# Optimization experiments

Measured on AMD Instinct MI355X. Metric: run time of the kernel, lower is better.

Reference implementation:

```python
import jax, jax.numpy as jnp
import numpy as np

MOD_EMBED_DIM = 16
HIDDEN = 64
NUM_MODALITIES = 3
MLP_IN = 2 + 2 * MOD_EMBED_DIM + 2  # 36


def setup_inputs() -> dict:
    key = jax.random.key(0)
    ks = jax.random.split(key, 4)
    h, w = 40, 40
    return {
        "h": h,
        "w": w,
        "q_mod": 0,
        "k_mod": 2,
        "structure_map": jax.random.normal(ks[0], (4, 1, 80, 80), jnp.float32),
        "mod_embed": jax.random.normal(ks[1], (NUM_MODALITIES, MOD_EMBED_DIM), jnp.float32),
        "W1": jax.random.normal(ks[2], (MLP_IN, HIDDEN), jnp.float32) * 0.1,
        "b1": jnp.zeros((HIDDEN,), jnp.float32),
        "W2": jax.random.normal(ks[3], (HIDDEN, 1), jnp.float32) * 0.1,
        "b2": jnp.zeros((1,), jnp.float32),
    }


def reference(h, w, q_mod, k_mod, structure_map, mod_embed, W1, b1, W2, b2):
    # --- coords on a [-0.5, 0.5] grid, flattened row-major -> (N, 2) as (x, y)
    ys = jnp.linspace(-0.5, 0.5, h)
    xs = jnp.linspace(-0.5, 0.5, w)
    yy, xx = jnp.meshgrid(ys, xs, indexing="ij")
    coords = jnp.stack([xx, yy], axis=-1).reshape(-1, 2)  # (N, 2)
    N = coords.shape[0]

    # relative coords per pair (i, j): (N, N, 2)
    rel = coords[:, None, :] - coords[None, :, :]

    # modality pair embedding: constant across all pairs -> (2*E,)
    mod_vec = jnp.concatenate([mod_embed[q_mod], mod_embed[k_mod]])

    # structure: bilinear resize to (h, w) (half-pixel == align_corners=False),
    # then mean over batch -> per-position scalar s_mean: (N,)
    b = structure_map.shape[0]
    s = jax.image.resize(structure_map, (b, 1, h, w), method="linear")
    s_mean = s.reshape(-1, 1, N)[:, 0, :].mean(axis=0)  # (N,)

    # First linear layer applied to the (implicit) concat
    # [rel, mod_vec, s_i, s_j] by splitting W1 — same math as concat @ W1,
    # but avoids materializing the (N^2, 36) concat tensor.
    W_rel = W1[:2]            # (2, H)
    W_mod = W1[2:2 + 2 * MOD_EMBED_DIM]  # (32, H)
    W_si = W1[-2]             # (H,)
    W_sj = W1[-1]             # (H,)

    hid = (
        jnp.einsum("ijc,ch->ijh", rel, W_rel)
        + (mod_vec @ W_mod + b1)
        + s_mean[:, None, None] * W_si
        + s_mean[None, :, None] * W_sj
    )  # (N, N, H)
    hid = jax.nn.relu(hid)
    bias = jnp.einsum("ijh,ho->ijo", hid, W2) + b2  # (N, N, 1)
    return bias.reshape(1, 1, N, N)
```

## Files before the change

kernel.cpp:

```cpp
#include <hip/hip_runtime.h>

#define HIN  80
#define WIN  80
#define NB   4
#define HOUT 40
#define WOUT 40
#define NPTS (HOUT*WOUT)
#define NHID 64

__global__ __launch_bounds__(64) void rpe_setup(
    const int* __restrict__ qmod, const int* __restrict__ kmod,
    const float* __restrict__ smap, const float* __restrict__ mode,
    const float* __restrict__ W1, const float* __restrict__ b1,
    float* __restrict__ Arows, float* __restrict__ Crows)
{
    __shared__ float wr0[NHID], wr1[NHID], wsi[NHID], wsj[NHID], sbase[NHID];
    __shared__ float smn[64], pxs[64], pys[64];
    const int t = threadIdx.x;

    wr0[t] = W1[t];
    wr1[t] = W1[NHID + t];
    wsi[t] = W1[34*NHID + t];
    wsj[t] = W1[35*NHID + t];
    const int q = qmod[0], k = kmod[0];
    float bacc = b1[t];
    #pragma unroll
    for (int m = 0; m < 16; ++m) bacc += mode[q*16 + m] * W1[(2 + m)*NHID + t];
    #pragma unroll
    for (int m = 0; m < 16; ++m) bacc += mode[k*16 + m] * W1[(18 + m)*NHID + t];
    sbase[t] = bacc;

    const int p  = blockIdx.x * 64 + t;
    const int oy = p / WOUT, ox = p % WOUT;
    float wy[4], wx[4]; int iy[4], ix[4];
    float wsy = 0.f, wsx = 0.f;
    #pragma unroll
    for (int d = 0; d < 4; ++d) {
        const float wv = (d == 0 || d == 3) ? 0.25f : 0.75f;
        const int yi = 2*oy + d - 1;
        const int xi = 2*ox + d - 1;
        iy[d] = yi < 0 ? 0 : (yi >= HIN ? HIN - 1 : yi);
        ix[d] = xi < 0 ? 0 : (xi >= WIN ? WIN - 1 : xi);
        wy[d] = (yi >= 0 && yi < HIN) ? wv : 0.f;
        wx[d] = (xi >= 0 && xi < WIN) ? wv : 0.f;
        wsy += wy[d]; wsx += wx[d];
    }
    float acc = 0.f;
    for (int b = 0; b < NB; ++b) {
        const float* bp = smap + b*HIN*WIN;
        #pragma unroll
        for (int dy = 0; dy < 4; ++dy) {
            const float* rp = bp + iy[dy]*WIN;
            float rs = 0.f;
            #pragma unroll
            for (int dx = 0; dx < 4; ++dx) rs += wx[dx] * rp[ix[dx]];
            acc += wy[dy] * rs;
        }
    }
    const float smean = acc / (wsy * wsx * (float)NB);
    smn[t] = smean;
    pxs[t] = -0.5f + (float)ox * (1.0f/(float)(WOUT-1));
    pys[t] = -0.5f + (float)oy * (1.0f/(float)(HOUT-1));
    __syncthreads();

    const float w0 = wr0[t], w1v = wr1[t], wiv = wsi[t], wjv = wsj[t], bb = sbase[t];
    const int pbase = blockIdx.x * 64;
    for (int pl = 0; pl < 64; ++pl) {
        const float lin = pxs[pl]*w0 + pys[pl]*w1v;
        const float s   = smn[pl];
        Arows[(pbase + pl)*NHID + t] =  lin + s*wiv + bb;
        Crows[(pbase + pl)*NHID + t] = -lin + s*wjv;
    }
}

__global__ __launch_bounds__(256) void rpe_bias(
    const float* __restrict__ Arows, const float* __restrict__ Crows,
    const float* __restrict__ W2, const float* __restrict__ b2,
    float* __restrict__ out)
{
    __shared__ float As[64][68];
    __shared__ float Cs[64][68];
    __shared__ float w2s[NHID];
    const int t  = threadIdx.x;
    const int bi = blockIdx.y, bj = blockIdx.x;

    #pragma unroll
    for (int k = 0; k < 4; ++k) {
        const int idx = t + k*256;
        const int row = idx >> 4;
        const int col = (idx & 15) << 2;
        const float4 av = *(const float4*)(Arows + (size_t)(bi*64 + row)*NHID + col);
        const float4 cv = *(const float4*)(Crows + (size_t)(bj*64 + row)*NHID + col);
        *(float4*)&As[row][col] = av;
        *(float4*)&Cs[row][col] = cv;
    }
    if (t < NHID) w2s[t] = W2[t];
    __syncthreads();

    const int tx = t & 15;
    const int ty = t >> 4;

    float4 acc[4][4];
    #pragma unroll
    for (int ii = 0; ii < 4; ++ii)
        #pragma unroll
        for (int jj = 0; jj < 4; ++jj) acc[ii][jj] = make_float4(0.f, 0.f, 0.f, 0.f);

    #pragma unroll
    for (int h = 0; h < NHID; h += 4) {
        const float4 w4 = *(const float4*)&w2s[h];
        float4 a[4], c[4];
        #pragma unroll
        for (int ii = 0; ii < 4; ++ii) a[ii] = *(const float4*)&As[ty + ii*16][h];
        #pragma unroll
        for (int jj = 0; jj < 4; ++jj) c[jj] = *(const float4*)&Cs[tx + jj*16][h];
        #pragma unroll
        for (int ii = 0; ii < 4; ++ii) {
            #pragma unroll
            for (int jj = 0; jj < 4; ++jj) {
                float4 v;
                v.x = fmaxf(a[ii].x + c[jj].x, 0.f);
                v.y = fmaxf(a[ii].y + c[jj].y, 0.f);
                v.z = fmaxf(a[ii].z + c[jj].z, 0.f);
                v.w = fmaxf(a[ii].w + c[jj].w, 0.f);
                acc[ii][jj].x = fmaf(v.x, w4.x, acc[ii][jj].x);
                acc[ii][jj].y = fmaf(v.y, w4.y, acc[ii][jj].y);
                acc[ii][jj].z = fmaf(v.z, w4.z, acc[ii][jj].z);
                acc[ii][jj].w = fmaf(v.w, w4.w, acc[ii][jj].w);
            }
        }
    }

    const float bias2 = b2[0];
    #pragma unroll
    for (int ii = 0; ii < 4; ++ii) {
        const int i = bi*64 + ty + ii*16;
        float* orow = out + (size_t)i*NPTS + bj*64;
        #pragma unroll
        for (int jj = 0; jj < 4; ++jj) {
            const float4 a4 = acc[ii][jj];
            orow[tx + jj*16] = (a4.x + a4.y) + (a4.z + a4.w) + bias2;
        }
    }
}

extern "C" void kernel_launch(void* const* d_in, const int* in_sizes, int n_in,
                              void* d_out, int out_size, void* d_ws, size_t ws_size,
                              hipStream_t stream) {
    const int*   qm   = (const int*)d_in[2];
    const int*   km   = (const int*)d_in[3];
    const float* smap = (const float*)d_in[4];
    const float* mode = (const float*)d_in[5];
    const float* W1   = (const float*)d_in[6];
    const float* b1   = (const float*)d_in[7];
    const float* W2   = (const float*)d_in[8];
    const float* b2   = (const float*)d_in[9];
    float* out = (float*)d_out;

    float* Arows = (float*)d_ws;
    float* Crows = Arows + (size_t)NPTS * NHID;

    rpe_setup<<<NPTS/64, 64, 0, stream>>>(qm, km, smap, mode, W1, b1, Arows, Crows);
    rpe_bias<<<dim3(NPTS/64, NPTS/64), 256, 0, stream>>>(Arows, Crows, W2, b2, out);
}
```

Baseline: 93.10 us.

## Fuse setup into bias kernel, recomputing A/C rows per tile in shared memory

Merges the setup kernel into the bias kernel. Each 64x64 tile block now computes its own resized structure means, coordinates and first-layer partial rows directly into shared memory, instead of reading precomputed A/C rows from a workspace. This removes one kernel launch and the global round trip through the workspace. In exchange, every block redundantly recomputes the bilinear resize and the modality bias, which adds gather loads of the structure map and extra prologue latency per block.

```diff
diff --git a/kernel.cpp b/kernel.cpp
--- a/kernel.cpp
+++ b/kernel.cpp
@@ -8,97 +8,90 @@
 #define NPTS (HOUT*WOUT)
 #define NHID 64
 
-__global__ __launch_bounds__(64) void rpe_setup(
+__global__ __launch_bounds__(256) void rpe_fused(
     const int* __restrict__ qmod, const int* __restrict__ kmod,
     const float* __restrict__ smap, const float* __restrict__ mode,
     const float* __restrict__ W1, const float* __restrict__ b1,
-    float* __restrict__ Arows, float* __restrict__ Crows)
-{
-    __shared__ float wr0[NHID], wr1[NHID], wsi[NHID], wsj[NHID], sbase[NHID];
-    __shared__ float smn[64], pxs[64], pys[64];
-    const int t = threadIdx.x;
-
-    wr0[t] = W1[t];
-    wr1[t] = W1[NHID + t];
-    wsi[t] = W1[34*NHID + t];
-    wsj[t] = W1[35*NHID + t];
-    const int q = qmod[0], k = kmod[0];
-    float bacc = b1[t];
-    #pragma unroll
-    for (int m = 0; m < 16; ++m) bacc += mode[q*16 + m] * W1[(2 + m)*NHID + t];
-    #pragma unroll
-    for (int m = 0; m < 16; ++m) bacc += mode[k*16 + m] * W1[(18 + m)*NHID + t];
-    sbase[t] = bacc;
-
-    const int p  = blockIdx.x * 64 + t;
-    const int oy = p / WOUT, ox = p % WOUT;
-    float wy[4], wx[4]; int iy[4], ix[4];
-    float wsy = 0.f, wsx = 0.f;
-    #pragma unroll
-    for (int d = 0; d < 4; ++d) {
-        const float wv = (d == 0 || d == 3) ? 0.25f : 0.75f;
-        const int yi = 2*oy + d - 1;
-        const int xi = 2*ox + d - 1;
-        iy[d] = yi < 0 ? 0 : (yi >= HIN ? HIN - 1 : yi);
-        ix[d] = xi < 0 ? 0 : (xi >= WIN ? WIN - 1 : xi);
-        wy[d] = (yi >= 0 && yi < HIN) ? wv : 0.f;
-        wx[d] = (xi >= 0 && xi < WIN) ? wv : 0.f;
-        wsy += wy[d]; wsx += wx[d];
-    }
-    float acc = 0.f;
-    for (int b = 0; b < NB; ++b) {
-        const float* bp = smap + b*HIN*WIN;
-        #pragma unroll
-        for (int dy = 0; dy < 4; ++dy) {
-            const float* rp = bp + iy[dy]*WIN;
-            float rs = 0.f;
-            #pragma unroll
-            for (int dx = 0; dx < 4; ++dx) rs += wx[dx] * rp[ix[dx]];
-            acc += wy[dy] * rs;
-        }
-    }
-    const float smean = acc / (wsy * wsx * (float)NB);
-    smn[t] = smean;
-    pxs[t] = -0.5f + (float)ox * (1.0f/(float)(WOUT-1));
-    pys[t] = -0.5f + (float)oy * (1.0f/(float)(HOUT-1));
-    __syncthreads();
-
-    const float w0 = wr0[t], w1v = wr1[t], wiv = wsi[t], wjv = wsj[t], bb = sbase[t];
-    const int pbase = blockIdx.x * 64;
-    for (int pl = 0; pl < 64; ++pl) {
-        const float lin = pxs[pl]*w0 + pys[pl]*w1v;
-        const float s   = smn[pl];
-        Arows[(pbase + pl)*NHID + t] =  lin + s*wiv + bb;
-        Crows[(pbase + pl)*NHID + t] = -lin + s*wjv;
-    }
-}
-
-__global__ __launch_bounds__(256) void rpe_bias(
-    const float* __restrict__ Arows, const float* __restrict__ Crows,
     const float* __restrict__ W2, const float* __restrict__ b2,
     float* __restrict__ out)
 {
     __shared__ float As[64][68];
     __shared__ float Cs[64][68];
-    __shared__ float w2s[NHID];
+    __shared__ float w0s[NHID], w1s[NHID], wis[NHID], wjs[NHID], bases[NHID], w2s[NHID];
+    __shared__ float sxi[64], syi[64], smi[64];
+    __shared__ float sxj[64], syj[64], smj[64];
+
     const int t  = threadIdx.x;
     const int bi = blockIdx.y, bj = blockIdx.x;
 
-    #pragma unroll
-    for (int k = 0; k < 4; ++k) {
-        const int idx = t + k*256;
-        const int row = idx >> 4;
-        const int col = (idx & 15) << 2;
-        const float4 av = *(const float4*)(Arows + (size_t)(bi*64 + row)*NHID + col);
-        const float4 cv = *(const float4*)(Crows + (size_t)(bj*64 + row)*NHID + col);
-        *(float4*)&As[row][col] = av;
-        *(float4*)&Cs[row][col] = cv;
+    if (t < 64) {
+        const int q = qmod[0], k = kmod[0];
+        w0s[t] = W1[t];
+        w1s[t] = W1[NHID + t];
+        wis[t] = W1[34*NHID + t];
+        wjs[t] = W1[35*NHID + t];
+        w2s[t] = W2[t];
+        float bacc = b1[t];
+        #pragma unroll
+        for (int m = 0; m < 16; ++m) bacc = fmaf(mode[q*16 + m], W1[(2 + m)*NHID + t], bacc);
+        #pragma unroll
+        for (int m = 0; m < 16; ++m) bacc = fmaf(mode[k*16 + m], W1[(18 + m)*NHID + t], bacc);
+        bases[t] = bacc;
+    } else if (t < 192) {
+        const int isJ = (t >= 128) ? 1 : 0;
+        const int idx = t - (isJ ? 128 : 64);
+        const int p   = (isJ ? bj : bi) * 64 + idx;
+        const int oy = p / WOUT, ox = p % WOUT;
+        float wy[4], wx[4]; int iy[4], ix[4];
+        float wsy = 0.f, wsx = 0.f;
+        #pragma unroll
+        for (int d = 0; d < 4; ++d) {
+            const float wv = (d == 0 || d == 3) ? 0.25f : 0.75f;
+            const int yi = 2*oy + d - 1;
+            const int xi = 2*ox + d - 1;
+            iy[d] = yi < 0 ? 0 : (yi >= HIN ? HIN - 1 : yi);
+            ix[d] = xi < 0 ? 0 : (xi >= WIN ? WIN - 1 : xi);
+            wy[d] = (yi >= 0 && yi < HIN) ? wv : 0.f;
+            wx[d] = (xi >= 0 && xi < WIN) ? wv : 0.f;
+            wsy += wy[d]; wsx += wx[d];
+        }
+        float acc = 0.f;
+        #pragma unroll
+        for (int b = 0; b < NB; ++b) {
+            const float* bp = smap + b*HIN*WIN;
+            #pragma unroll
+            for (int dy = 0; dy < 4; ++dy) {
+                const float* rp = bp + iy[dy]*WIN;
+                float rs = 0.f;
+                #pragma unroll
+                for (int dx = 0; dx < 4; ++dx) rs = fmaf(wx[dx], rp[ix[dx]], rs);
+                acc = fmaf(wy[dy], rs, acc);
+            }
+        }
+        const float sm = acc / (wsy * wsx * (float)NB);
+        const float x = -0.5f + (float)ox * (1.0f/(float)(WOUT-1));
+        const float y = -0.5f + (float)oy * (1.0f/(float)(HOUT-1));
+        if (isJ) { sxj[idx] = x; syj[idx] = y; smj[idx] = sm; }
+        else     { sxi[idx] = x; syi[idx] = y; smi[idx] = sm; }
     }
-    if (t < NHID) w2s[t] = W2[t];
+    __syncthreads();
+
+    {
+        const int h = t & 63;
+        const int g = t >> 6;
+        const float w0 = w0s[h], w1v = w1s[h], wiv = wis[h], wjv = wjs[h], bb = bases[h];
+        #pragma unroll
+        for (int r = 0; r < 16; ++r) {
+            const int row = g*16 + r;
+            As[row][h] = fmaf(sxi[row], w0, fmaf(syi[row], w1v, fmaf(smi[row], wiv, bb)));
+            Cs[row][h] = fmaf(smj[row], wjv, -fmaf(sxj[row], w0, syj[row] * w1v));
+        }
+    }
     __syncthreads();
 
     const int tx = t & 15;
     const int ty = t >> 4;
+    const float bias2 = b2[0];
 
     float4 acc[4][4];
     #pragma unroll
@@ -131,7 +124,6 @@
         }
     }
 
-    const float bias2 = b2[0];
     #pragma unroll
     for (int ii = 0; ii < 4; ++ii) {
         const int i = bi*64 + ty + ii*16;
@@ -156,10 +148,8 @@
     const float* W2   = (const float*)d_in[8];
     const float* b2   = (const float*)d_in[9];
     float* out = (float*)d_out;
+    (void)d_ws; (void)ws_size;
 
-    float* Arows = (float*)d_ws;
-    float* Crows = Arows + (size_t)NPTS * NHID;
-
-    rpe_setup<<<NPTS/64, 64, 0, stream>>>(qm, km, smap, mode, W1, b1, Arows, Crows);
-    rpe_bias<<<dim3(NPTS/64, NPTS/64), 256, 0, stream>>>(Arows, Crows, W2, b2, out);
+    rpe_fused<<<dim3(NPTS/64, NPTS/64), 256, 0, stream>>>(
+        qm, km, smap, mode, W1, b1, W2, b2, out);
 }
```

New measurement: 90.49 us. -2.8%, faster.
